# Optimization experiments

Measured on AMD Instinct MI355X. Metric: run time of the kernel, lower is better.

Reference implementation:

```python
import jax, jax.numpy as jnp
import numpy as np

D_MODEL = 512
NUM_HEADS = 8
HEAD_DIM = D_MODEL // NUM_HEADS
MAX_REL = 2


def setup_inputs() -> dict:
    key = jax.random.key(0)
    ks = jax.random.split(key, 12)
    B, S = 2, 4096
    std = 1.0 / np.sqrt(D_MODEL)
    inp = {
        'q': jax.random.normal(ks[0], (B, S, D_MODEL), jnp.float32),
        'k': jax.random.normal(ks[1], (B, S, D_MODEL), jnp.float32),
        'v': jax.random.normal(ks[2], (B, S, D_MODEL), jnp.float32),
        'Wq': jax.random.normal(ks[3], (D_MODEL, D_MODEL), jnp.float32) * std,
        'bq': jnp.zeros((D_MODEL,), jnp.float32),
        'Wk': jax.random.normal(ks[4], (D_MODEL, D_MODEL), jnp.float32) * std,
        'bk': jnp.zeros((D_MODEL,), jnp.float32),
        'Wv': jax.random.normal(ks[5], (D_MODEL, D_MODEL), jnp.float32) * std,
        'bv': jnp.zeros((D_MODEL,), jnp.float32),
        'Wo': jax.random.normal(ks[6], (D_MODEL, D_MODEL), jnp.float32) * std,
        'bo': jnp.zeros((D_MODEL,), jnp.float32),
        'rel_pos': jax.random.normal(ks[7], (NUM_HEADS, 2 * MAX_REL + 1), jnp.float32),
    }
    return inp


def _rel_bias(rel_pos, seq_len):
    pos = jnp.arange(seq_len)
    rel = pos[None, :] - pos[:, None]              # [S,S]
    idx = jnp.clip(rel, -MAX_REL, MAX_REL) + MAX_REL
    return rel_pos[:, idx]                         # [H,S,S]


def reference(q, k, v, Wq, bq, Wk, bk, Wv, bv, Wo, bo, rel_pos):
    B, S, D = q.shape
    H, Hd = NUM_HEADS, HEAD_DIM
    # torch Linear: x @ W.T + b
    Q = (q @ Wq.T + bq).reshape(B, S, H, Hd).transpose(0, 2, 1, 3)  # [B,H,S,Hd]
    K = (k @ Wk.T + bk).reshape(B, S, H, Hd).transpose(0, 2, 1, 3)
    V = (v @ Wv.T + bv).reshape(B, S, H, Hd).transpose(0, 2, 1, 3)
    scores = jnp.einsum('bhqd,bhkd->bhqk', Q, K) / jnp.sqrt(jnp.float32(Hd))
    scores = scores + _rel_bias(rel_pos, S)[None]                  # [B,H,S,S]
    probs = jax.nn.softmax(scores, axis=-1)
    attn = jnp.einsum('bhqk,bhkd->bhqd', probs, V)                 # [B,H,S,Hd]
    attn = attn.transpose(0, 2, 1, 3).reshape(B, S, D)
    return attn @ Wo.T + bo
```

## Files before the change

### kernel.cpp

```cpp
#include <hip/hip_runtime.h>

typedef __bf16 bf16_t;
typedef __bf16 bf16x4 __attribute__((ext_vector_type(4)));
typedef __bf16 bf16x8 __attribute__((ext_vector_type(8)));
typedef float f32x4 __attribute__((ext_vector_type(4)));

#define MFMA16(a, b, c) __builtin_amdgcn_mfma_f32_16x16x32_bf16(a, b, c, 0, 0, 0)
#define LOG2E 1.4426950408889634f

#define GLL(g, l)                                                      \
  __builtin_amdgcn_global_load_lds(                                    \
      (const __attribute__((address_space(1))) void*)(g),              \
      (__attribute__((address_space(3))) void*)(l), 16, 0, 0)

static constexpr int NB = 2;
static constexpr int SEQ = 4096;
static constexpr int DM = 512;
static constexpr int NH = 8;
static constexpr int HD = 64;
static constexpr int M_ROWS = NB * SEQ;

__global__ __launch_bounds__(256) void cvt_w_kernel(
    const float* __restrict__ w0, const float* __restrict__ w1,
    const float* __restrict__ w2, const float* __restrict__ w3,
    bf16_t* __restrict__ out) {
  const float* src = (blockIdx.y == 0) ? w0 : (blockIdx.y == 1) ? w1
                   : (blockIdx.y == 2) ? w2 : w3;
  int i = (blockIdx.x * 256 + threadIdx.x) * 4;
  float4 v = *(const float4*)(src + i);
  bf16_t* o = out + blockIdx.y * (DM * DM) + i;
  o[0] = (bf16_t)v.x; o[1] = (bf16_t)v.y; o[2] = (bf16_t)v.z; o[3] = (bf16_t)v.w;
}

template <int XMODE, int TM>
__device__ __forceinline__ void gemm_body(
    const void* __restrict__ Xv, const bf16_t* __restrict__ Wm,
    const float* __restrict__ bias, void* __restrict__ Out,
    int omode, float scale) {
  constexpr int MB = TM / 32;
  __shared__ bf16_t Asm[TM * 32];
  __shared__ bf16_t Bsm[128 * 32];

  const int tid = threadIdx.x;
  const int w = tid >> 6;
  const int lane = tid & 63;
  const int quad = lane >> 4, l15 = lane & 15;
  const int m0 = blockIdx.x * TM;
  const int n0 = blockIdx.y * 128;
  const int moff = (w & 1) * (TM / 2);
  const int noff = (w >> 1) * 64;

  const float* Xf = (const float*)Xv;
  const bf16_t* Xb = (const bf16_t*)Xv;

  f32x4 acc[MB][4];
#pragma unroll
  for (int mb = 0; mb < MB; mb++)
#pragma unroll
    for (int nb = 0; nb < 4; nb++) { acc[mb][nb][0] = 0.f; acc[mb][nb][1] = 0.f; acc[mb][nb][2] = 0.f; acc[mb][nb][3] = 0.f; }

  for (int k0 = 0; k0 < DM; k0 += 32) {
    __syncthreads();
#pragma unroll
    for (int j = 0; j < 2; j++) {
      const int c = w * 64 + lane + j * 256;
      GLL(Wm + (size_t)(n0 + (c >> 2)) * DM + k0 + (c & 3) * 8,
          Bsm + (w * 64 + j * 256) * 8);
    }
    if (XMODE == 1) {
#pragma unroll
      for (int j = 0; j < TM * 32 / 2048; j++) {
        const int c = w * 64 + lane + j * 256;
        GLL(Xb + (size_t)(m0 + (c >> 2)) * DM + k0 + (c & 3) * 8,
            Asm + (w * 64 + j * 256) * 8);
      }
    } else {
      const int arow = tid >> 1;
      const int aseg = (tid & 1) * 16;
      const float* src = Xf + (size_t)(m0 + arow) * DM + k0 + aseg;
      float4 x0 = *(const float4*)(src);
      float4 x1 = *(const float4*)(src + 4);
      float4 x2 = *(const float4*)(src + 8);
      float4 x3 = *(const float4*)(src + 12);
      bf16x8 p0, p1;
      p0[0] = (bf16_t)x0.x; p0[1] = (bf16_t)x0.y; p0[2] = (bf16_t)x0.z; p0[3] = (bf16_t)x0.w;
      p0[4] = (bf16_t)x1.x; p0[5] = (bf16_t)x1.y; p0[6] = (bf16_t)x1.z; p0[7] = (bf16_t)x1.w;
      p1[0] = (bf16_t)x2.x; p1[1] = (bf16_t)x2.y; p1[2] = (bf16_t)x2.z; p1[3] = (bf16_t)x2.w;
      p1[4] = (bf16_t)x3.x; p1[5] = (bf16_t)x3.y; p1[6] = (bf16_t)x3.z; p1[7] = (bf16_t)x3.w;
      *(bf16x8*)&Asm[arow * 32 + aseg] = p0;
      *(bf16x8*)&Asm[arow * 32 + aseg + 8] = p1;
    }
    __syncthreads();

    bf16x8 bfr[4];
#pragma unroll
    for (int nb = 0; nb < 4; nb++)
      bfr[nb] = *(const bf16x8*)&Bsm[(noff + nb * 16 + l15) * 32 + 8 * quad];
#pragma unroll
    for (int mb = 0; mb < MB; mb++) {
      bf16x8 a = *(const bf16x8*)&Asm[(moff + mb * 16 + l15) * 32 + 8 * quad];
#pragma unroll
      for (int nb = 0; nb < 4; nb++) acc[mb][nb] = MFMA16(a, bfr[nb], acc[mb][nb]);
    }
  }

#pragma unroll
  for (int nb = 0; nb < 4; nb++) {
    const int n = n0 + noff + nb * 16 + l15;
    const float bn = bias[n];
    const int h = n >> 6, dd = n & 63;
#pragma unroll
    for (int mb = 0; mb < MB; mb++) {
      const int mbase = m0 + moff + mb * 16 + quad * 4;
      const int bb = mbase >> 12, s = mbase & 4095;
      if (omode == 0) {
#pragma unroll
        for (int r = 0; r < 4; r++) {
          const float val = (acc[mb][nb][r] + bn) * scale;
          ((bf16_t*)Out)[(size_t)((bb * NH + h) * SEQ + s + r) * HD + dd] = (bf16_t)val;
        }
      } else if (omode == 1) {
        bf16x4 pk;
#pragma unroll
        for (int r = 0; r < 4; r++) pk[r] = (bf16_t)(acc[mb][nb][r] + bn);
        *(bf16x4*)&((bf16_t*)Out)[(((size_t)(bb * NH + h) * HD + dd) << 12) + s] = pk;
      } else {
#pragma unroll
        for (int r = 0; r < 4; r++)
          ((float*)Out)[(size_t)(mbase + r) * DM + n] = acc[mb][nb][r] + bn;
      }
    }
  }
}

__global__ __launch_bounds__(256, 3) void qkv_kernel(
    const float* __restrict__ q, const float* __restrict__ k,
    const float* __restrict__ v, const bf16_t* __restrict__ Wall,
    const float* __restrict__ bq, const float* __restrict__ bk,
    const float* __restrict__ bv, bf16_t* __restrict__ Qb,
    bf16_t* __restrict__ Kb, bf16_t* __restrict__ Vb, float qscale) {
  const int z = blockIdx.z;
  const float* X = (z == 0) ? q : (z == 1) ? k : v;
  const float* bias = (z == 0) ? bq : (z == 1) ? bk : bv;
  bf16_t* Out = (z == 0) ? Qb : (z == 1) ? Kb : Vb;
  gemm_body<0, 128>(X, Wall + (size_t)z * DM * DM, bias, Out,
                    (z == 2) ? 1 : 0, (z == 0) ? qscale : 1.0f);
}

__global__ __launch_bounds__(256, 3) void oproj_kernel(
    const bf16_t* __restrict__ X, const bf16_t* __restrict__ Wm,
    const float* __restrict__ bias, float* __restrict__ Out) {
  gemm_body<1, 64>(X, Wm, bias, Out, 2, 1.0f);
}

__global__ __launch_bounds__(256, 2) void attn_kernel(
    const bf16_t* __restrict__ Qb, const bf16_t* __restrict__ Kb,
    const bf16_t* __restrict__ Vb, const float* __restrict__ rel_pos,
    bf16_t* __restrict__ attn_out) {
  __shared__ bf16_t Kt[64 * 64];
  __shared__ bf16_t Vt[64 * 64];
  __shared__ bf16_t Pt[4][32 * 72];

  const int w = threadIdx.x >> 6;
  const int lane = threadIdx.x & 63;
  const int quad = lane >> 4, l15 = lane & 15;
  const int bh = blockIdx.y;
  const int b = bh >> 3, h = bh & 7;
  const int qlo = blockIdx.x * 128 + w * 32;

  const float rb0 = rel_pos[h * 5 + 0] * LOG2E;
  const float rb1 = rel_pos[h * 5 + 1] * LOG2E;
  const float rb2 = rel_pos[h * 5 + 2] * LOG2E;
  const float rb3 = rel_pos[h * 5 + 3] * LOG2E;
  const float rb4 = rel_pos[h * 5 + 4] * LOG2E;

  bf16x8 qf[2][2];
#pragma unroll
  for (int mb = 0; mb < 2; mb++)
#pragma unroll
    for (int kd = 0; kd < 2; kd++)
      qf[mb][kd] = *(const bf16x8*)(Qb + (size_t)(bh * SEQ + qlo + mb * 16 + l15) * HD + kd * 32 + 8 * quad);

  f32x4 o[2][4];
#pragma unroll
  for (int mb = 0; mb < 2; mb++)
#pragma unroll
    for (int db = 0; db < 4; db++) { o[mb][db][0] = 0.f; o[mb][db][1] = 0.f; o[mb][db][2] = 0.f; o[mb][db][3] = 0.f; }
  f32x4 l4[2];
  l4[0][0] = 0.f; l4[0][1] = 0.f; l4[0][2] = 0.f; l4[0][3] = 0.f;
  l4[1][0] = 0.f; l4[1][1] = 0.f; l4[1][2] = 0.f; l4[1][3] = 0.f;

  bf16x8 ones;
#pragma unroll
  for (int i = 0; i < 8; i++) ones[i] = (bf16_t)1.0f;

  const int srow = (w << 4) + (lane >> 3);
  const int scol = (((lane & 7) ^ (lane >> 3)) << 3);
  const bf16_t* kg0 = Kb + ((size_t)(bh * SEQ + srow) << 6) + scol;
  const bf16_t* kg1 = kg0 + (8 << 6);
  const bf16_t* vg0 = Vb + ((size_t)(bh * HD + srow) << 12) + scol;
  const bf16_t* vg1 = vg0 + (8 << 12);
  bf16_t* kl0 = Kt + (w << 10);
  bf16_t* kl1 = kl0 + 512;
  bf16_t* vl0 = Vt + (w << 10);
  bf16_t* vl1 = vl0 + 512;

  const int swz = l15 & 7;
  const bf16_t* kf0 = Kt + (l15 << 6) + (((quad    ) ^ swz) << 3);
  const bf16_t* kf1 = Kt + (l15 << 6) + (((quad + 4) ^ swz) << 3);
  const bf16_t* vf0 = Vt + (l15 << 6) + (((quad    ) ^ swz) << 3);
  const bf16_t* vf1 = Vt + (l15 << 6) + (((quad + 4) ^ swz) << 3);

  for (int t = 0; t < 64; t++) {
    const int kk0 = t * 64;
    __syncthreads();
    GLL(kg0 + (t << 12), kl0);
    GLL(kg1 + (t << 12), kl1);
    GLL(vg0 + (t << 6), vl0);
    GLL(vg1 + (t << 6), vl1);
    __syncthreads();

    float cini;
    bool nearband = false;
    if (kk0 >= qlo + 33) {
      cini = rb4 - 16.0f;
    } else if (kk0 + 63 <= qlo - 2) {
      cini = rb0 - 16.0f;
    } else {
      cini = -16.0f;
      nearband = true;
    }

    f32x4 s[2][4];
#pragma unroll
    for (int mb = 0; mb < 2; mb++)
#pragma unroll
      for (int kb = 0; kb < 4; kb++) { s[mb][kb][0] = cini; s[mb][kb][1] = cini; s[mb][kb][2] = cini; s[mb][kb][3] = cini; }
#pragma unroll
    for (int kb = 0; kb < 4; kb++) {
      bf16x8 kA0 = *(const bf16x8*)(kf0 + (kb << 10));
      bf16x8 kA1 = *(const bf16x8*)(kf1 + (kb << 10));
      s[0][kb] = MFMA16(kA0, qf[0][0], s[0][kb]);
      s[0][kb] = MFMA16(kA1, qf[0][1], s[0][kb]);
      s[1][kb] = MFMA16(kA0, qf[1][0], s[1][kb]);
      s[1][kb] = MFMA16(kA1, qf[1][1], s[1][kb]);
    }

    if (nearband) {
#pragma unroll
      for (int mb = 0; mb < 2; mb++) {
        const int qg = qlo + mb * 16 + l15;
#pragma unroll
        for (int kb = 0; kb < 4; kb++)
#pragma unroll
          for (int r = 0; r < 4; r++) {
            int dl = kk0 + kb * 16 + quad * 4 + r - qg;
            float bias = dl <= -2 ? rb0
                       : (dl >= 2 ? rb4
                       : (dl == -1 ? rb1 : (dl == 0 ? rb2 : rb3)));
            s[mb][kb][r] += bias;
          }
      }
    }

#pragma unroll
    for (int mb = 0; mb < 2; mb++) {
      bf16_t* Pr = &Pt[w][(mb * 16 + l15) * 72];
#pragma unroll
      for (int kb = 0; kb < 4; kb++) {
        bf16x4 pk;
#pragma unroll
        for (int r = 0; r < 4; r++)
          pk[r] = (bf16_t)__builtin_amdgcn_exp2f(s[mb][kb][r]);
        *(bf16x4*)&Pr[kb * 16 + quad * 4] = pk;
      }
    }

    bf16x8 pf[2][2];
#pragma unroll
    for (int mb = 0; mb < 2; mb++)
#pragma unroll
      for (int kc = 0; kc < 2; kc++)
        pf[mb][kc] = *(const bf16x8*)&Pt[w][(mb * 16 + l15) * 72 + kc * 32 + quad * 8];

    l4[0] = MFMA16(ones, pf[0][0], l4[0]);
    l4[0] = MFMA16(ones, pf[0][1], l4[0]);
    l4[1] = MFMA16(ones, pf[1][0], l4[1]);
    l4[1] = MFMA16(ones, pf[1][1], l4[1]);

#pragma unroll
    for (int db = 0; db < 4; db++) {
      bf16x8 vA0 = *(const bf16x8*)(vf0 + (db << 10));
      bf16x8 vA1 = *(const bf16x8*)(vf1 + (db << 10));
      o[0][db] = MFMA16(vA0, pf[0][0], o[0][db]);
      o[0][db] = MFMA16(vA1, pf[0][1], o[0][db]);
      o[1][db] = MFMA16(vA0, pf[1][0], o[1][db]);
      o[1][db] = MFMA16(vA1, pf[1][1], o[1][db]);
    }
  }

#pragma unroll
  for (int mb = 0; mb < 2; mb++) {
    const float inv = 1.0f / l4[mb][0];
    const int qg = qlo + mb * 16 + l15;
#pragma unroll
    for (int db = 0; db < 4; db++) {
      bf16x4 pk;
#pragma unroll
      for (int r = 0; r < 4; r++) pk[r] = (bf16_t)(o[mb][db][r] * inv);
      *(bf16x4*)(attn_out + (size_t)(b * SEQ + qg) * DM + h * HD + db * 16 + quad * 4) = pk;
    }
  }
}

extern "C" void kernel_launch(void* const* d_in, const int* in_sizes, int n_in,
                              void* d_out, int out_size, void* d_ws, size_t ws_size,
                              hipStream_t stream) {
  const float* q   = (const float*)d_in[0];
  const float* k   = (const float*)d_in[1];
  const float* v   = (const float*)d_in[2];
  const float* Wq  = (const float*)d_in[3];
  const float* bq  = (const float*)d_in[4];
  const float* Wk  = (const float*)d_in[5];
  const float* bk  = (const float*)d_in[6];
  const float* Wv  = (const float*)d_in[7];
  const float* bv  = (const float*)d_in[8];
  const float* Wo  = (const float*)d_in[9];
  const float* bo  = (const float*)d_in[10];
  const float* rel = (const float*)d_in[11];

  char* ws = (char*)d_ws;
  bf16_t* Wbf  = (bf16_t*)ws;
  bf16_t* Qbuf = (bf16_t*)(ws + (size_t)(2  << 20));
  bf16_t* Kbuf = (bf16_t*)(ws + (size_t)(10 << 20));
  bf16_t* Vbuf = (bf16_t*)(ws + (size_t)(18 << 20));
  bf16_t* Abuf = (bf16_t*)(ws + (size_t)(26 << 20));

  cvt_w_kernel<<<dim3(256, 4), 256, 0, stream>>>(Wq, Wk, Wv, Wo, Wbf);

  const float qscale = LOG2E / 8.0f;
  qkv_kernel<<<dim3(64, 4, 3), 256, 0, stream>>>(
      q, k, v, Wbf, bq, bk, bv, Qbuf, Kbuf, Vbuf, qscale);

  attn_kernel<<<dim3(32, 16), 256, 0, stream>>>(Qbuf, Kbuf, Vbuf, rel, Abuf);

  oproj_kernel<<<dim3(128, 4), 256, 0, stream>>>(Abuf, Wbf + 3 * DM * DM, bo, (float*)d_out);
}
```

Before: 241.3 us.

## Double-buffer LDS tiles in GEMMs and attention with swizzled layouts

Both projection GEMMs move to a shared 64-row tile body with K-step 64. They double-buffer LDS so the next tile's global loads (and the fp32-to-bf16 conversion of X) overlap the current MFMA work, and they use XOR-swizzled LDS columns to avoid bank conflicts. The attention kernel prefetches the next K/V tile into a second LDS buffer, cutting two barriers per iteration to one, and swaps the padded P scratch for a swizzled unpadded layout. The QKV grid doubles to match the smaller tile, at the cost of more LDS per block, which may lower occupancy.

```diff
diff --git a/kernel.cpp b/kernel.cpp
--- a/kernel.cpp
+++ b/kernel.cpp
@@ -7,6 +7,7 @@
 
 #define MFMA16(a, b, c) __builtin_amdgcn_mfma_f32_16x16x32_bf16(a, b, c, 0, 0, 0)
 #define LOG2E 1.4426950408889634f
+#define SHIFT 16.0f
 
 #define GLL(g, l)                                                      \
   __builtin_amdgcn_global_load_lds(                                    \
@@ -32,76 +33,118 @@
   o[0] = (bf16_t)v.x; o[1] = (bf16_t)v.y; o[2] = (bf16_t)v.z; o[3] = (bf16_t)v.w;
 }
 
-template <int XMODE, int TM>
-__device__ __forceinline__ void gemm_body(
+template <int XMODE>
+__device__ __forceinline__ void gemm_body64(
     const void* __restrict__ Xv, const bf16_t* __restrict__ Wm,
     const float* __restrict__ bias, void* __restrict__ Out,
     int omode, float scale) {
-  constexpr int MB = TM / 32;
-  __shared__ bf16_t Asm[TM * 32];
-  __shared__ bf16_t Bsm[128 * 32];
+  __shared__ bf16_t Asm[2][64 * 64];
+  __shared__ bf16_t Bsm[2][128 * 64];
 
   const int tid = threadIdx.x;
   const int w = tid >> 6;
   const int lane = tid & 63;
   const int quad = lane >> 4, l15 = lane & 15;
-  const int m0 = blockIdx.x * TM;
+  const int l8 = lane >> 3;
+  const int swcol = ((lane & 7) ^ (l8 & 7)) * 8;
+  const int m0 = blockIdx.x * 64;
   const int n0 = blockIdx.y * 128;
-  const int moff = (w & 1) * (TM / 2);
+  const int moff = (w & 1) * 32;
   const int noff = (w >> 1) * 64;
 
+  const bf16_t* Xb = (const bf16_t*)Xv;
   const float* Xf = (const float*)Xv;
-  const bf16_t* Xb = (const bf16_t*)Xv;
-
-  f32x4 acc[MB][4];
-#pragma unroll
-  for (int mb = 0; mb < MB; mb++)
+
+  const int arow = tid >> 2;
+  const int aseg = (tid & 3) * 16;
+  const int ach = (tid & 3) * 2;
+  const int asw = arow & 7;
+
+  f32x4 acc[2][4];
+#pragma unroll
+  for (int mb = 0; mb < 2; mb++)
 #pragma unroll
     for (int nb = 0; nb < 4; nb++) { acc[mb][nb][0] = 0.f; acc[mb][nb][1] = 0.f; acc[mb][nb][2] = 0.f; acc[mb][nb][3] = 0.f; }
 
-  for (int k0 = 0; k0 < DM; k0 += 32) {
+#pragma unroll
+  for (int j = 0; j < 4; j++) {
+    const int row = j * 32 + w * 8 + l8;
+    GLL(Wm + (size_t)(n0 + row) * DM + swcol, &Bsm[0][(j * 256 + w * 64) * 8]);
+  }
+  if (XMODE == 1) {
+#pragma unroll
+    for (int j = 0; j < 2; j++) {
+      const int row = j * 32 + w * 8 + l8;
+      GLL(Xb + (size_t)(m0 + row) * DM + swcol, &Asm[0][(j * 256 + w * 64) * 8]);
+    }
+  } else {
+    const float* src = Xf + (size_t)(m0 + arow) * DM + aseg;
+    float4 x0 = *(const float4*)(src);
+    float4 x1 = *(const float4*)(src + 4);
+    float4 x2 = *(const float4*)(src + 8);
+    float4 x3 = *(const float4*)(src + 12);
+    bf16x8 p0, p1;
+    p0[0] = (bf16_t)x0.x; p0[1] = (bf16_t)x0.y; p0[2] = (bf16_t)x0.z; p0[3] = (bf16_t)x0.w;
+    p0[4] = (bf16_t)x1.x; p0[5] = (bf16_t)x1.y; p0[6] = (bf16_t)x1.z; p0[7] = (bf16_t)x1.w;
+    p1[0] = (bf16_t)x2.x; p1[1] = (bf16_t)x2.y; p1[2] = (bf16_t)x2.z; p1[3] = (bf16_t)x2.w;
+    p1[4] = (bf16_t)x3.x; p1[5] = (bf16_t)x3.y; p1[6] = (bf16_t)x3.z; p1[7] = (bf16_t)x3.w;
+    *(bf16x8*)&Asm[0][arow * 64 + ((ach ^ asw) * 8)] = p0;
+    *(bf16x8*)&Asm[0][arow * 64 + (((ach + 1) ^ asw) * 8)] = p1;
+  }
+  __syncthreads();
+
+  for (int ks = 0; ks < 8; ks++) {
+    const int p = ks & 1, pn = p ^ 1;
+    float4 xr0, xr1, xr2, xr3;
+    if (ks < 7) {
+      const int k0n = (ks + 1) * 64;
+      if (XMODE == 0) {
+        const float* src = Xf + (size_t)(m0 + arow) * DM + k0n + aseg;
+        xr0 = *(const float4*)(src);
+        xr1 = *(const float4*)(src + 4);
+        xr2 = *(const float4*)(src + 8);
+        xr3 = *(const float4*)(src + 12);
+      } else {
+#pragma unroll
+        for (int j = 0; j < 2; j++) {
+          const int row = j * 32 + w * 8 + l8;
+          GLL(Xb + (size_t)(m0 + row) * DM + k0n + swcol,
+              &Asm[pn][(j * 256 + w * 64) * 8]);
+        }
+      }
+#pragma unroll
+      for (int j = 0; j < 4; j++) {
+        const int row = j * 32 + w * 8 + l8;
+        GLL(Wm + (size_t)(n0 + row) * DM + k0n + swcol,
+            &Bsm[pn][(j * 256 + w * 64) * 8]);
+      }
+    }
+
+#pragma unroll
+    for (int kd = 0; kd < 2; kd++) {
+      const int fch = (((kd << 2) + quad) ^ (l15 & 7)) << 3;
+      bf16x8 bfr[4];
+#pragma unroll
+      for (int nb = 0; nb < 4; nb++)
+        bfr[nb] = *(const bf16x8*)&Bsm[p][(noff + nb * 16 + l15) * 64 + fch];
+#pragma unroll
+      for (int mb = 0; mb < 2; mb++) {
+        bf16x8 a = *(const bf16x8*)&Asm[p][(moff + mb * 16 + l15) * 64 + fch];
+#pragma unroll
+        for (int nb = 0; nb < 4; nb++) acc[mb][nb] = MFMA16(a, bfr[nb], acc[mb][nb]);
+      }
+    }
+
+    if (XMODE == 0 && ks < 7) {
+      bf16x8 p0, p1;
+      p0[0] = (bf16_t)xr0.x; p0[1] = (bf16_t)xr0.y; p0[2] = (bf16_t)xr0.z; p0[3] = (bf16_t)xr0.w;
+      p0[4] = (bf16_t)xr1.x; p0[5] = (bf16_t)xr1.y; p0[6] = (bf16_t)xr1.z; p0[7] = (bf16_t)xr1.w;
+      p1[0] = (bf16_t)xr2.x; p1[1] = (bf16_t)xr2.y; p1[2] = (bf16_t)xr2.z; p1[3] = (bf16_t)xr2.w;
+      p1[4] = (bf16_t)xr3.x; p1[5] = (bf16_t)xr3.y; p1[6] = (bf16_t)xr3.z; p1[7] = (bf16_t)xr3.w;
+      *(bf16x8*)&Asm[pn][arow * 64 + ((ach ^ asw) * 8)] = p0;
+      *(bf16x8*)&Asm[pn][arow * 64 + (((ach + 1) ^ asw) * 8)] = p1;
+    }
     __syncthreads();
-#pragma unroll
-    for (int j = 0; j < 2; j++) {
-      const int c = w * 64 + lane + j * 256;
-      GLL(Wm + (size_t)(n0 + (c >> 2)) * DM + k0 + (c & 3) * 8,
-          Bsm + (w * 64 + j * 256) * 8);
-    }
-    if (XMODE == 1) {
-#pragma unroll
-      for (int j = 0; j < TM * 32 / 2048; j++) {
-        const int c = w * 64 + lane + j * 256;
-        GLL(Xb + (size_t)(m0 + (c >> 2)) * DM + k0 + (c & 3) * 8,
-            Asm + (w * 64 + j * 256) * 8);
-      }
-    } else {
-      const int arow = tid >> 1;
-      const int aseg = (tid & 1) * 16;
-      const float* src = Xf + (size_t)(m0 + arow) * DM + k0 + aseg;
-      float4 x0 = *(const float4*)(src);
-      float4 x1 = *(const float4*)(src + 4);
-      float4 x2 = *(const float4*)(src + 8);
-      float4 x3 = *(const float4*)(src + 12);
-      bf16x8 p0, p1;
-      p0[0] = (bf16_t)x0.x; p0[1] = (bf16_t)x0.y; p0[2] = (bf16_t)x0.z; p0[3] = (bf16_t)x0.w;
-      p0[4] = (bf16_t)x1.x; p0[5] = (bf16_t)x1.y; p0[6] = (bf16_t)x1.z; p0[7] = (bf16_t)x1.w;
-      p1[0] = (bf16_t)x2.x; p1[1] = (bf16_t)x2.y; p1[2] = (bf16_t)x2.z; p1[3] = (bf16_t)x2.w;
-      p1[4] = (bf16_t)x3.x; p1[5] = (bf16_t)x3.y; p1[6] = (bf16_t)x3.z; p1[7] = (bf16_t)x3.w;
-      *(bf16x8*)&Asm[arow * 32 + aseg] = p0;
-      *(bf16x8*)&Asm[arow * 32 + aseg + 8] = p1;
-    }
-    __syncthreads();
-
-    bf16x8 bfr[4];
-#pragma unroll
-    for (int nb = 0; nb < 4; nb++)
-      bfr[nb] = *(const bf16x8*)&Bsm[(noff + nb * 16 + l15) * 32 + 8 * quad];
-#pragma unroll
-    for (int mb = 0; mb < MB; mb++) {
-      bf16x8 a = *(const bf16x8*)&Asm[(moff + mb * 16 + l15) * 32 + 8 * quad];
-#pragma unroll
-      for (int nb = 0; nb < 4; nb++) acc[mb][nb] = MFMA16(a, bfr[nb], acc[mb][nb]);
-    }
   }
 
 #pragma unroll
@@ -110,7 +153,7 @@
     const float bn = bias[n];
     const int h = n >> 6, dd = n & 63;
 #pragma unroll
-    for (int mb = 0; mb < MB; mb++) {
+    for (int mb = 0; mb < 2; mb++) {
       const int mbase = m0 + moff + mb * 16 + quad * 4;
       const int bb = mbase >> 12, s = mbase & 4095;
       if (omode == 0) {
@@ -143,26 +186,27 @@
   const float* X = (z == 0) ? q : (z == 1) ? k : v;
   const float* bias = (z == 0) ? bq : (z == 1) ? bk : bv;
   bf16_t* Out = (z == 0) ? Qb : (z == 1) ? Kb : Vb;
-  gemm_body<0, 128>(X, Wall + (size_t)z * DM * DM, bias, Out,
-                    (z == 2) ? 1 : 0, (z == 0) ? qscale : 1.0f);
+  gemm_body64<0>(X, Wall + (size_t)z * DM * DM, bias, Out,
+                 (z == 2) ? 1 : 0, (z == 0) ? qscale : 1.0f);
 }
 
 __global__ __launch_bounds__(256, 3) void oproj_kernel(
     const bf16_t* __restrict__ X, const bf16_t* __restrict__ Wm,
     const float* __restrict__ bias, float* __restrict__ Out) {
-  gemm_body<1, 64>(X, Wm, bias, Out, 2, 1.0f);
+  gemm_body64<1>(X, Wm, bias, Out, 2, 1.0f);
 }
 
 __global__ __launch_bounds__(256, 2) void attn_kernel(
     const bf16_t* __restrict__ Qb, const bf16_t* __restrict__ Kb,
     const bf16_t* __restrict__ Vb, const float* __restrict__ rel_pos,
     bf16_t* __restrict__ attn_out) {
-  __shared__ bf16_t Kt[64 * 64];
-  __shared__ bf16_t Vt[64 * 64];
-  __shared__ bf16_t Pt[4][32 * 72];
-
-  const int w = threadIdx.x >> 6;
-  const int lane = threadIdx.x & 63;
+  __shared__ bf16_t Kt[2][64 * 64];
+  __shared__ bf16_t Vt[2][64 * 64];
+  __shared__ bf16_t Pt[4][32 * 64];
+
+  const int tid = threadIdx.x;
+  const int w = tid >> 6;
+  const int lane = tid & 63;
   const int quad = lane >> 4, l15 = lane & 15;
   const int bh = blockIdx.y;
   const int b = bh >> 3, h = bh & 7;
@@ -197,37 +241,37 @@
   const int srow = (w << 4) + (lane >> 3);
   const int scol = (((lane & 7) ^ (lane >> 3)) << 3);
   const bf16_t* kg0 = Kb + ((size_t)(bh * SEQ + srow) << 6) + scol;
-  const bf16_t* kg1 = kg0 + (8 << 6);
-  const bf16_t* vg0 = Vb + ((size_t)(bh * HD + srow) << 12) + scol;
-  const bf16_t* vg1 = vg0 + (8 << 12);
-  bf16_t* kl0 = Kt + (w << 10);
-  bf16_t* kl1 = kl0 + 512;
-  bf16_t* vl0 = Vt + (w << 10);
-  bf16_t* vl1 = vl0 + 512;
-
-  const int swz = l15 & 7;
-  const bf16_t* kf0 = Kt + (l15 << 6) + (((quad    ) ^ swz) << 3);
-  const bf16_t* kf1 = Kt + (l15 << 6) + (((quad + 4) ^ swz) << 3);
-  const bf16_t* vf0 = Vt + (l15 << 6) + (((quad    ) ^ swz) << 3);
-  const bf16_t* vf1 = Vt + (l15 << 6) + (((quad + 4) ^ swz) << 3);
+  const bf16_t* vg0 = Vb + (((size_t)(bh * HD + srow)) << 12) + scol;
+  const int ldst = (w << 10);
+
+  const int sw = l15 & 7;
+  const int kfo0 = (l15 << 6) + ((quad ^ sw) << 3);
+  const int kfo1 = (l15 << 6) + (((quad + 4) ^ sw) << 3);
+
+  GLL(kg0, &Kt[0][ldst]);
+  GLL(kg0 + (8 << 6), &Kt[0][ldst + 512]);
+  GLL(vg0, &Vt[0][ldst]);
+  GLL(vg0 + (8 << 12), &Vt[0][ldst + 512]);
+  __syncthreads();
 
   for (int t = 0; t < 64; t++) {
+    const int p = t & 1, pn = p ^ 1;
     const int kk0 = t * 64;
-    __syncthreads();
-    GLL(kg0 + (t << 12), kl0);
-    GLL(kg1 + (t << 12), kl1);
-    GLL(vg0 + (t << 6), vl0);
-    GLL(vg1 + (t << 6), vl1);
-    __syncthreads();
+
+    const int tg = (t < 63) ? t + 1 : 63;
+    GLL(kg0 + ((size_t)tg << 12), &Kt[pn][ldst]);
+    GLL(kg0 + ((size_t)tg << 12) + (8 << 6), &Kt[pn][ldst + 512]);
+    GLL(vg0 + (tg << 6), &Vt[pn][ldst]);
+    GLL(vg0 + (tg << 6) + (8 << 12), &Vt[pn][ldst + 512]);
 
     float cini;
     bool nearband = false;
     if (kk0 >= qlo + 33) {
-      cini = rb4 - 16.0f;
+      cini = rb4 - SHIFT;
     } else if (kk0 + 63 <= qlo - 2) {
-      cini = rb0 - 16.0f;
+      cini = rb0 - SHIFT;
     } else {
-      cini = -16.0f;
+      cini = -SHIFT;
       nearband = true;
     }
 
@@ -238,8 +282,8 @@
       for (int kb = 0; kb < 4; kb++) { s[mb][kb][0] = cini; s[mb][kb][1] = cini; s[mb][kb][2] = cini; s[mb][kb][3] = cini; }
 #pragma unroll
     for (int kb = 0; kb < 4; kb++) {
-      bf16x8 kA0 = *(const bf16x8*)(kf0 + (kb << 10));
-      bf16x8 kA1 = *(const bf16x8*)(kf1 + (kb << 10));
+      bf16x8 kA0 = *(const bf16x8*)&Kt[p][kfo0 + (kb << 10)];
+      bf16x8 kA1 = *(const bf16x8*)&Kt[p][kfo1 + (kb << 10)];
       s[0][kb] = MFMA16(kA0, qf[0][0], s[0][kb]);
       s[0][kb] = MFMA16(kA1, qf[0][1], s[0][kb]);
       s[1][kb] = MFMA16(kA0, qf[1][0], s[1][kb]);
@@ -265,14 +309,14 @@
 
 #pragma unroll
     for (int mb = 0; mb < 2; mb++) {
-      bf16_t* Pr = &Pt[w][(mb * 16 + l15) * 72];
+      bf16_t* Pr = &Pt[w][(mb * 16 + l15) * 64];
 #pragma unroll
       for (int kb = 0; kb < 4; kb++) {
         bf16x4 pk;
 #pragma unroll
         for (int r = 0; r < 4; r++)
           pk[r] = (bf16_t)__builtin_amdgcn_exp2f(s[mb][kb][r]);
-        *(bf16x4*)&Pr[kb * 16 + quad * 4] = pk;
+        *(bf16x4*)&Pr[(((kb * 2 + (quad >> 1)) ^ sw) << 3) + ((quad & 1) << 2)] = pk;
       }
     }
 
@@ -281,7 +325,7 @@
     for (int mb = 0; mb < 2; mb++)
 #pragma unroll
       for (int kc = 0; kc < 2; kc++)
-        pf[mb][kc] = *(const bf16x8*)&Pt[w][(mb * 16 + l15) * 72 + kc * 32 + quad * 8];
+        pf[mb][kc] = *(const bf16x8*)&Pt[w][(mb * 16 + l15) * 64 + ((((kc << 2) + quad) ^ sw) << 3)];
 
     l4[0] = MFMA16(ones, pf[0][0], l4[0]);
     l4[0] = MFMA16(ones, pf[0][1], l4[0]);
@@ -290,13 +334,15 @@
 
 #pragma unroll
     for (int db = 0; db < 4; db++) {
-      bf16x8 vA0 = *(const bf16x8*)(vf0 + (db << 10));
-      bf16x8 vA1 = *(const bf16x8*)(vf1 + (db << 10));
+      bf16x8 vA0 = *(const bf16x8*)&Vt[p][kfo0 + (db << 10)];
+      bf16x8 vA1 = *(const bf16x8*)&Vt[p][kfo1 + (db << 10)];
       o[0][db] = MFMA16(vA0, pf[0][0], o[0][db]);
       o[0][db] = MFMA16(vA1, pf[0][1], o[0][db]);
       o[1][db] = MFMA16(vA0, pf[1][0], o[1][db]);
       o[1][db] = MFMA16(vA1, pf[1][1], o[1][db]);
     }
+
+    __syncthreads();
   }
 
 #pragma unroll
@@ -339,7 +385,7 @@
   cvt_w_kernel<<<dim3(256, 4), 256, 0, stream>>>(Wq, Wk, Wv, Wo, Wbf);
 
   const float qscale = LOG2E / 8.0f;
-  qkv_kernel<<<dim3(64, 4, 3), 256, 0, stream>>>(
+  qkv_kernel<<<dim3(128, 4, 3), 256, 0, stream>>>(
       q, k, v, Wbf, bq, bk, bv, Qbuf, Kbuf, Vbuf, qscale);
 
   attn_kernel<<<dim3(32, 16), 256, 0, stream>>>(Qbuf, Kbuf, Vbuf, rel, Abuf);
```

Result: no change. 240.8 us (-0.2%).
